# Kernel tuning notes

Measured on AMD Instinct MI355X. Metric: run time of the kernel, lower is better.

The kernel has to match this reference:

```python
import jax, jax.numpy as jnp
import numpy as np

NUM_ITERATIONS = 3
NUM_SLOTS = 8
SLOT_SIZE = 256
MLP_HIDDEN = 512
EPSILON = 1e-8
LN_EPS = 1e-5


def _ln(x, w, b):
    m = jnp.mean(x, axis=-1, keepdims=True)
    v = jnp.var(x, axis=-1, keepdims=True)
    return (x - m) * jax.lax.rsqrt(v + LN_EPS) * w + b


def _gru_cell(x, h, w_ih, w_hh, b_ih, b_hh):
    # torch.nn.GRUCell semantics; gates ordered [r, z, n]
    gi = x @ w_ih.T + b_ih
    gh = h @ w_hh.T + b_hh
    ir, iz, inn = jnp.split(gi, 3, axis=-1)
    hr, hz, hn = jnp.split(gh, 3, axis=-1)
    r = jax.nn.sigmoid(ir + hr)
    z = jax.nn.sigmoid(iz + hz)
    n = jnp.tanh(inn + r * hn)
    return (1.0 - z) * n + z * h


def setup_inputs() -> dict:
    key = jax.random.key(0)
    ks = jax.random.split(key, 12)
    D, H = SLOT_SIZE, MLP_HIDDEN
    s = 0.02
    return {
        "inputs": jax.random.normal(ks[0], (64, 4096, D), dtype=jnp.float32),
        "noise": jax.random.normal(ks[1], (64, NUM_SLOTS, D), dtype=jnp.float32),
        "ln_in_w": jnp.ones((D,), jnp.float32), "ln_in_b": jnp.zeros((D,), jnp.float32),
        "ln_slots_w": jnp.ones((D,), jnp.float32), "ln_slots_b": jnp.zeros((D,), jnp.float32),
        "ln_mlp_w": jnp.ones((D,), jnp.float32), "ln_mlp_b": jnp.zeros((D,), jnp.float32),
        "slots_mu": jax.random.normal(ks[2], (1, 1, D), jnp.float32) * s,
        "slots_log_sigma": jnp.zeros((1, 1, D), jnp.float32),
        "Wq": jax.random.normal(ks[3], (D, D), jnp.float32) * s,
        "Wk": jax.random.normal(ks[4], (D, D), jnp.float32) * s,
        "Wv": jax.random.normal(ks[5], (D, D), jnp.float32) * s,
        "gru_w_ih": jax.random.normal(ks[6], (3 * D, D), jnp.float32) * s,
        "gru_w_hh": jax.random.normal(ks[7], (3 * D, D), jnp.float32) * s,
        "gru_b_ih": jnp.zeros((3 * D,), jnp.float32),
        "gru_b_hh": jnp.zeros((3 * D,), jnp.float32),
        "mlp_w1": jax.random.normal(ks[8], (H, D), jnp.float32) * s,
        "mlp_b1": jnp.zeros((H,), jnp.float32),
        "mlp_w2": jax.random.normal(ks[9], (D, H), jnp.float32) * s,
        "mlp_b2": jnp.zeros((D,), jnp.float32),
    }


def reference(inputs, noise, ln_in_w, ln_in_b, ln_slots_w, ln_slots_b, ln_mlp_w, ln_mlp_b,
              slots_mu, slots_log_sigma, Wq, Wk, Wv,
              gru_w_ih, gru_w_hh, gru_b_ih, gru_b_hh,
              mlp_w1, mlp_b1, mlp_w2, mlp_b2):
    B, N, D = inputs.shape
    S = NUM_SLOTS
    x = _ln(inputs, ln_in_w, ln_in_b)            # [B,N,D]
    k = x @ Wk.T                                  # [B,N,D]
    v = x @ Wv.T                                  # [B,N,D]
    slots = slots_mu + jnp.exp(slots_log_sigma) * noise   # [B,S,D]
    scale = D ** (-0.5)
    for _ in range(NUM_ITERATIONS):
        slots_prev = slots
        s_n = _ln(slots, ln_slots_w, ln_slots_b)
        q = (s_n @ Wq.T) * scale                  # [B,S,D]
        attn_logits = jnp.einsum('bnd,bsd->bns', k, q)
        attn = jax.nn.softmax(attn_logits, axis=-1) + EPSILON
        attn = attn / jnp.sum(attn, axis=-2, keepdims=True)   # renorm over inputs
        updates = jnp.einsum('bns,bnd->bsd', attn, v)          # [B,S,D]
        slots = _gru_cell(updates.reshape(-1, D), slots_prev.reshape(-1, D),
                          gru_w_ih, gru_w_hh, gru_b_ih, gru_b_hh).reshape(B, S, D)
        h = jax.nn.relu(_ln(slots, ln_mlp_w, ln_mlp_b) @ mlp_w1.T + mlp_b1)
        slots = slots + (h @ mlp_w2.T + mlp_b2)
    return slots
```

## Files before the change

kernel.cpp:

```cpp
#include <hip/hip_runtime.h>

#define CB 64
#define CN 4096
#define CD 256
#define CS 8
#define CH 512

typedef __bf16 bf16_t;
typedef bf16_t bf16x8 __attribute__((ext_vector_type(8)));
typedef float f32x4 __attribute__((ext_vector_type(4)));

__device__ __forceinline__ unsigned short f2bf(float f){
  unsigned int u = __builtin_bit_cast(unsigned int, f);
  u += 0x7FFFu + ((u >> 16) & 1u);
  return (unsigned short)(u >> 16);
}

__device__ __forceinline__ f32x4 mfma16(bf16x8 a, bf16x8 b, f32x4 c){
  return __builtin_amdgcn_mfma_f32_16x16x32_bf16(a, b, c, 0, 0, 0);
}

__device__ __forceinline__ void gl_lds16(const void* g, void* l){
  __builtin_amdgcn_global_load_lds(
      (const __attribute__((address_space(1))) unsigned int*)g,
      (__attribute__((address_space(3))) unsigned int*)l, 16, 0, 0);
}

__global__ __launch_bounds__(256) void k_ln(const float* __restrict__ in,
    const float* __restrict__ gw, const float* __restrict__ gb,
    unsigned short* __restrict__ x){
  int blk = blockIdx.x;
  int b = blk >> 6, nt = blk & 63;
  int wv = threadIdx.x >> 6, l = threadIdx.x & 63;
  const float* base = in + ((size_t)b*CN + (size_t)nt*64) * CD;
  unsigned short* xb = x + ((size_t)b*CN + (size_t)nt*64) * CD;
  float4 w4 = *(const float4*)(gw + 4*l);
  float4 b4 = *(const float4*)(gb + 4*l);
  for(int i = 0; i < 16; i++){
    int r = wv*16 + i;
    float4 v = *(const float4*)(base + (size_t)r*CD + 4*l);
    float s1 = v.x + v.y + v.z + v.w;
    float s2 = v.x*v.x + v.y*v.y + v.z*v.z + v.w*v.w;
    #pragma unroll
    for(int m = 1; m < 64; m <<= 1){ s1 += __shfl_xor(s1, m); s2 += __shfl_xor(s2, m); }
    float mean = s1 * (1.0f/CD);
    float var  = fmaxf(s2 * (1.0f/CD) - mean*mean, 0.0f);
    float rstd = rsqrtf(var + 1e-5f);
    float y0 = (v.x - mean)*rstd*w4.x + b4.x;
    float y1 = (v.y - mean)*rstd*w4.y + b4.y;
    float y2 = (v.z - mean)*rstd*w4.z + b4.z;
    float y3 = (v.w - mean)*rstd*w4.w + b4.w;
    uint2 p;
    p.x = (unsigned)f2bf(y0) | ((unsigned)f2bf(y1) << 16);
    p.y = (unsigned)f2bf(y2) | ((unsigned)f2bf(y3) << 16);
    *(uint2*)(xb + (size_t)r*CD + 4*l) = p;
  }
}

__global__ __launch_bounds__(256) void k_setup(
    const float* __restrict__ Wq, const float* __restrict__ Wk,
    const float* __restrict__ wih, const float* __restrict__ Wv,
    const float* __restrict__ whh, const float* __restrict__ w1,
    const float* __restrict__ w2, const float* __restrict__ noise,
    const float* __restrict__ mu, const float* __restrict__ lsig,
    unsigned short* __restrict__ M1T, unsigned short* __restrict__ Mih_bf,
    unsigned short* __restrict__ Whh_bf, unsigned short* __restrict__ w1_bf,
    unsigned short* __restrict__ w2_bf, float* __restrict__ slots){
  int bid = blockIdx.x, tid = threadIdx.x;
  if(bid < 256){
    int ep = bid, e = tid;
    float acc = 0.0f;
    for(int d = 0; d < 256; d++) acc = fmaf(Wq[(size_t)d*256 + e], Wk[(size_t)d*256 + ep], acc);
    M1T[(size_t)ep*256 + e] = f2bf(acc * 0.0625f);
  } else if(bid < 1024){
    int j = bid - 256, e = tid;
    float acc = 0.0f;
    for(int d = 0; d < 256; d++) acc = fmaf(wih[(size_t)j*256 + d], Wv[(size_t)d*256 + e], acc);
    Mih_bf[(size_t)j*256 + e] = f2bf(acc);
  } else if(bid < 1792){
    int idx = (bid - 1024)*256 + tid;
    Whh_bf[idx] = f2bf(whh[idx]);
  } else if(bid < 2304){
    int idx = (bid - 1792)*256 + tid;
    w1_bf[idx] = f2bf(w1[idx]);
  } else if(bid < 2816){
    int idx = (bid - 2304)*256 + tid;
    w2_bf[idx] = f2bf(w2[idx]);
  } else {
    int idx = (bid - 2816)*256 + tid;
    int d = idx & 255;
    slots[idx] = mu[d] + __expf(lsig[d]) * noise[idx];
  }
}

__global__ __launch_bounds__(256) void k_attn(const unsigned short* __restrict__ x,
    const float* __restrict__ slots, const float* __restrict__ lsw,
    const float* __restrict__ lsb, const unsigned short* __restrict__ M1T,
    float* __restrict__ Upart, float* __restrict__ dpart){
  __shared__ unsigned short xt[64*256];
  __shared__ unsigned short pt[16*72];
  __shared__ float dred[4][8];
  int b = blockIdx.x >> 4, chunk = blockIdx.x & 15;
  int tid = threadIdx.x;
  int wv = tid >> 6, l = tid & 63;
  int lm = l & 15, lg = l >> 4;

  unsigned short* sn    = xt;
  unsigned short* qtile = xt + 4224;
  {
    float4 w4 = *(const float4*)(lsw + 4*l);
    float4 b4 = *(const float4*)(lsb + 4*l);
    for(int i = 0; i < 2; i++){
      int r = wv*2 + i;
      float4 v = *(const float4*)(slots + ((size_t)b*CS + r)*CD + 4*l);
      float s1 = v.x + v.y + v.z + v.w;
      float s2 = v.x*v.x + v.y*v.y + v.z*v.z + v.w*v.w;
      #pragma unroll
      for(int m = 1; m < 64; m <<= 1){ s1 += __shfl_xor(s1, m); s2 += __shfl_xor(s2, m); }
      float mean = s1 * (1.0f/CD);
      float var  = fmaxf(s2 * (1.0f/CD) - mean*mean, 0.0f);
      float rstd = rsqrtf(var + 1e-5f);
      float y0 = (v.x - mean)*rstd*w4.x + b4.x;
      float y1 = (v.y - mean)*rstd*w4.y + b4.y;
      float y2 = (v.z - mean)*rstd*w4.z + b4.z;
      float y3 = (v.w - mean)*rstd*w4.w + b4.w;
      uint2 p;
      p.x = (unsigned)f2bf(y0) | ((unsigned)f2bf(y1) << 16);
      p.y = (unsigned)f2bf(y2) | ((unsigned)f2bf(y3) << 16);
      *(uint2*)(&sn[r*264 + 4*l]) = p;
      uint2 zz; zz.x = 0u; zz.y = 0u;
      *(uint2*)(&sn[(r+8)*264 + 4*l]) = zz;
    }
    __syncthreads();
    bf16x8 af[8];
    #pragma unroll
    for(int k = 0; k < 8; k++) af[k] = *(const bf16x8*)(&sn[lm*264 + k*32 + lg*8]);
    #pragma unroll
    for(int ntile = 0; ntile < 4; ntile++){
      int ep = wv*64 + ntile*16 + lm;
      f32x4 acc = {0.f, 0.f, 0.f, 0.f};
      const unsigned short* mrow = M1T + (size_t)ep*CD;
      #pragma unroll
      for(int k = 0; k < 8; k++){
        bf16x8 bf = *(const bf16x8*)(mrow + k*32 + lg*8);
        acc = mfma16(af[k], bf, acc);
      }
      #pragma unroll
      for(int reg = 0; reg < 4; reg++)
        qtile[(lg*4 + reg)*264 + ep] = f2bf(acc[reg]);
    }
    __syncthreads();
  }
  bf16x8 qb[8];
  #pragma unroll
  for(int k = 0; k < 8; k++) qb[k] = *(const bf16x8*)(&qtile[lm*264 + k*32 + lg*8]);

  f32x4 uacc[4];
  #pragma unroll
  for(int nt = 0; nt < 4; nt++){ f32x4 z = {0.f,0.f,0.f,0.f}; uacc[nt] = z; }
  float dacc = 0.0f;

  const unsigned short* xbatch = x + (size_t)b*CN*CD + (size_t)chunk*256*CD;

  for(int t = 0; t < 4; t++){
    const unsigned short* xtile = xbatch + (size_t)t*64*CD;
    __syncthreads();
    #pragma unroll
    for(int k2 = 0; k2 < 8; k2++){
      int r0 = wv*16 + k2*2;
      int row = r0 + (l >> 5);
      int c = l & 31;
      int f = (row ^ (row >> 3)) & 7;
      const unsigned short* g = xtile + (size_t)row*CD + (size_t)(c ^ f)*8;
      gl_lds16(g, &xt[r0*CD]);
    }
    __syncthreads();

    f32x4 c4 = {0.f, 0.f, 0.f, 0.f};
    int rowl = wv*16 + lm;
    int f1 = (rowl ^ (rowl >> 3)) & 7;
    #pragma unroll
    for(int k = 0; k < 8; k++){
      int cc = (k*4 + lg) ^ f1;
      bf16x8 a = *(const bf16x8*)(&xt[rowl*256 + cc*8]);
      c4 = mfma16(a, qb[k], c4);
    }
    float pv[4];
    #pragma unroll
    for(int reg = 0; reg < 4; reg++){
      float v = (lm < 8) ? c4[reg] : -1e30f;
      float mx = v;
      #pragma unroll
      for(int m = 1; m < 16; m <<= 1) mx = fmaxf(mx, __shfl_xor(mx, m));
      float e = __expf(v - mx);
      float s = e;
      #pragma unroll
      for(int m = 1; m < 16; m <<= 1) s += __shfl_xor(s, m);
      float p = (lm < 8) ? (e/s + 1e-8f) : 0.0f;
      dacc += p;
      pv[reg] = p;
    }
    int rbase = wv*16 + lg*4;
    unsigned int p01 = (unsigned)f2bf(pv[0]) | ((unsigned)f2bf(pv[1]) << 16);
    unsigned int p23 = (unsigned)f2bf(pv[2]) | ((unsigned)f2bf(pv[3]) << 16);
    *(unsigned int*)(&pt[lm*72 + rbase])     = p01;
    *(unsigned int*)(&pt[lm*72 + rbase + 2]) = p23;
    __syncthreads();

    #pragma unroll
    for(int ks = 0; ks < 2; ks++){
      bf16x8 a = *(const bf16x8*)(&pt[lm*72 + ks*32 + lg*8]);
      int rb = ks*32 + lg*8;
      #pragma unroll
      for(int nt = 0; nt < 4; nt++){
        int e = wv*64 + nt*16 + lm;
        bf16x8 bfr;
        #pragma unroll
        for(int j = 0; j < 8; j++){
          int row2 = rb + j;
          int f2 = (row2 ^ (row2 >> 3)) & 7;
          int cidx = (e >> 3) ^ f2;
          unsigned short tv = xt[row2*256 + cidx*8 + (e & 7)];
          bfr[j] = __builtin_bit_cast(bf16_t, tv);
        }
        uacc[nt] = mfma16(a, bfr, uacc[nt]);
      }
    }
  }

  dacc += __shfl_xor(dacc, 16);
  dacc += __shfl_xor(dacc, 32);
  if(l < 8) dred[wv][l] = dacc;
  if(lg < 2){
    float* Ub = Upart + (((size_t)chunk*CB + b)*CS)*CD;
    #pragma unroll
    for(int nt = 0; nt < 4; nt++){
      #pragma unroll
      for(int reg = 0; reg < 4; reg++){
        int s = lg*4 + reg;
        Ub[(size_t)s*CD + wv*64 + nt*16 + lm] = uacc[nt][reg];
      }
    }
  }
  __syncthreads();
  if(tid < 8)
    dpart[((size_t)chunk*CB + b)*CS + tid] =
        dred[0][tid] + dred[1][tid] + dred[2][tid] + dred[3][tid];
}

__global__ __launch_bounds__(512) void k_update(
    const float* __restrict__ Upart, const float* slots,
    const float* __restrict__ dpart,
    const unsigned short* __restrict__ Mih, const unsigned short* __restrict__ Whh,
    const unsigned short* __restrict__ w1b, const unsigned short* __restrict__ w2b,
    const float* __restrict__ bih, const float* __restrict__ bhh,
    const float* __restrict__ lmw, const float* __restrict__ lmb,
    const float* __restrict__ b1, const float* __restrict__ b2,
    float* out){
  __shared__ unsigned short A1[16*264];
  __shared__ unsigned short SBf[16*264];
  __shared__ unsigned short A3[16*520];
  __shared__ float G1[8*777];
  __shared__ float G2[8*777];
  __shared__ float Hh[8*257];
  int b = blockIdx.x, tid = threadIdx.x;
  int l = tid & 63, lm = l & 15, lg = l >> 4;
  int wv = tid >> 6;

  for(int i = tid; i < 8*264; i += 512){ A1[8*264 + i] = 0; SBf[8*264 + i] = 0; }
  for(int i = tid; i < 8*520; i += 512) A3[8*520 + i] = 0;
  if(tid < 256){
    int r = tid >> 5, c = (tid & 31)*8;
    float s0=0.f,s1=0.f,s2=0.f,s3=0.f,s4=0.f,s5=0.f,s6=0.f,s7=0.f;
    #pragma unroll
    for(int ch = 0; ch < 16; ch++){
      const float* Up = Upart + (((size_t)ch*CB + b)*CS + r)*CD + c;
      float4 a0 = *(const float4*)Up;
      float4 a1 = *(const float4*)(Up + 4);
      s0 += a0.x; s1 += a0.y; s2 += a0.z; s3 += a0.w;
      s4 += a1.x; s5 += a1.y; s6 += a1.z; s7 += a1.w;
    }
    uint4 pk;
    pk.x = (unsigned)f2bf(s0) | ((unsigned)f2bf(s1) << 16);
    pk.y = (unsigned)f2bf(s2) | ((unsigned)f2bf(s3) << 16);
    pk.z = (unsigned)f2bf(s4) | ((unsigned)f2bf(s5) << 16);
    pk.w = (unsigned)f2bf(s6) | ((unsigned)f2bf(s7) << 16);
    *(uint4*)(&A1[r*264 + c]) = pk;
  } else {
    int t2 = tid & 255;
    int r = t2 >> 5, c = (t2 & 31)*8;
    const float* src = slots + ((size_t)b*CS + r)*CD + c;
    float4 a0 = *(const float4*)src, a1 = *(const float4*)(src + 4);
    uint4 pk;
    pk.x = (unsigned)f2bf(a0.x) | ((unsigned)f2bf(a0.y) << 16);
    pk.y = (unsigned)f2bf(a0.z) | ((unsigned)f2bf(a0.w) << 16);
    pk.z = (unsigned)f2bf(a1.x) | ((unsigned)f2bf(a1.y) << 16);
    pk.w = (unsigned)f2bf(a1.z) | ((unsigned)f2bf(a1.w) << 16);
    *(uint4*)(&SBf[r*264 + c]) = pk;
  }
  __syncthreads();

  {
    const unsigned short* W = (wv < 4) ? Mih : Whh;
    const unsigned short* As = (wv < 4) ? A1 : SBf;
    float* G = (wv < 4) ? G1 : G2;
    int w4 = wv & 3;
    bf16x8 af[8];
    #pragma unroll
    for(int k = 0; k < 8; k++) af[k] = *(const bf16x8*)(&As[lm*264 + k*32 + lg*8]);
    const unsigned short* brow = W + ((size_t)(w4*192 + lm))*CD + lg*8;
    bf16x8 bv[8], bw[8];
    #pragma unroll
    for(int k = 0; k < 8; k++) bv[k] = *(const bf16x8*)(brow + k*32);
    for(int t = 0; t < 12; t++){
      if(t < 11){
        const unsigned short* bn = brow + (size_t)(t + 1)*16*CD;
        #pragma unroll
        for(int k = 0; k < 8; k++) bw[k] = *(const bf16x8*)(bn + k*32);
      }
      f32x4 acc = {0.f,0.f,0.f,0.f};
      #pragma unroll
      for(int k = 0; k < 8; k++) acc = mfma16(af[k], bv[k], acc);
      if(lg < 2){
        int cb = w4*192 + t*16 + lm;
        #pragma unroll
        for(int reg = 0; reg < 4; reg++) G[(lg*4 + reg)*777 + cb] = acc[reg];
      }
      #pragma unroll
      for(int k = 0; k < 8; k++) bv[k] = bw[k];
    }
  }
  __syncthreads();

  {
    int r = wv;
    float dsum = dpart[((size_t)(l & 15)*CB + b)*CS + r];
    #pragma unroll
    for(int m = 1; m < 16; m <<= 1) dsum += __shfl_xor(dsum, m);
    float invd = 1.0f / dsum;
    const float* srow = slots + ((size_t)b*CS + r)*CD;
    float hv[4]; float s1 = 0.f, s2 = 0.f;
    #pragma unroll
    for(int i = 0; i < 4; i++){
      int c = l + 64*i;
      float gr = G1[r*777 + c]*invd + bih[c] + G2[r*777 + c] + bhh[c];
      float gz = G1[r*777 + 256 + c]*invd + bih[256 + c] + G2[r*777 + 256 + c] + bhh[256 + c];
      float gn = G1[r*777 + 512 + c]*invd + bih[512 + c];
      float hn = G2[r*777 + 512 + c] + bhh[512 + c];
      float rr = 1.0f/(1.0f + __expf(-gr));
      float zz = 1.0f/(1.0f + __expf(-gz));
      float nn = tanhf(gn + rr*hn);
      float h = (1.0f - zz)*nn + zz*srow[c];
      hv[i] = h; Hh[r*257 + c] = h; s1 += h; s2 += h*h;
    }
    #pragma unroll
    for(int m = 1; m < 64; m <<= 1){ s1 += __shfl_xor(s1, m); s2 += __shfl_xor(s2, m); }
    float mean = s1 * (1.0f/CD);
    float var  = fmaxf(s2 * (1.0f/CD) - mean*mean, 0.0f);
    float rstd = rsqrtf(var + 1e-5f);
    #pragma unroll
    for(int i = 0; i < 4; i++){
      int c = l + 64*i;
      A1[r*264 + c] = f2bf((hv[i] - mean)*rstd*lmw[c] + lmb[c]);
    }
  }
  __syncthreads();

  {
    bf16x8 af[8];
    #pragma unroll
    for(int k = 0; k < 8; k++) af[k] = *(const bf16x8*)(&A1[lm*264 + k*32 + lg*8]);
    const unsigned short* brow = w1b + ((size_t)(wv*64 + lm))*CD + lg*8;
    for(int t = 0; t < 4; t++){
      const unsigned short* bn = brow + (size_t)t*16*CD;
      f32x4 acc = {0.f,0.f,0.f,0.f};
      #pragma unroll
      for(int k = 0; k < 8; k++){
        bf16x8 bv = *(const bf16x8*)(bn + k*32);
        acc = mfma16(af[k], bv, acc);
      }
      if(lg < 2){
        int c = wv*64 + t*16 + lm;
        float bb = b1[c];
        #pragma unroll
        for(int reg = 0; reg < 4; reg++)
          A3[(lg*4 + reg)*520 + c] = f2bf(fmaxf(acc[reg] + bb, 0.0f));
      }
    }
  }
  __syncthreads();

  {
    bf16x8 af[16];
    #pragma unroll
    for(int k = 0; k < 16; k++) af[k] = *(const bf16x8*)(&A3[lm*520 + k*32 + lg*8]);
    const unsigned short* brow = w2b + ((size_t)(wv*32 + lm))*CH + lg*8;
    for(int t = 0; t < 2; t++){
      const unsigned short* bn = brow + (size_t)t*16*CH;
      f32x4 acc = {0.f,0.f,0.f,0.f};
      #pragma unroll
      for(int k = 0; k < 16; k++){
        bf16x8 bv = *(const bf16x8*)(bn + k*32);
        acc = mfma16(af[k], bv, acc);
      }
      if(lg < 2){
        int c = wv*32 + t*16 + lm;
        float bb = b2[c];
        #pragma unroll
        for(int reg = 0; reg < 4; reg++){
          int row = lg*4 + reg;
          out[((size_t)b*CS + row)*CD + c] = acc[reg] + bb + Hh[row*257 + c];
        }
      }
    }
  }
}

extern "C" void kernel_launch(void* const* d_in, const int* in_sizes, int n_in,
                              void* d_out, int out_size, void* d_ws, size_t ws_size,
                              hipStream_t stream){
  const float* inputs = (const float*)d_in[0];
  const float* noise  = (const float*)d_in[1];
  const float* ln_in_w = (const float*)d_in[2];
  const float* ln_in_b = (const float*)d_in[3];
  const float* ln_sl_w = (const float*)d_in[4];
  const float* ln_sl_b = (const float*)d_in[5];
  const float* ln_ml_w = (const float*)d_in[6];
  const float* ln_ml_b = (const float*)d_in[7];
  const float* mu   = (const float*)d_in[8];
  const float* lsig = (const float*)d_in[9];
  const float* Wq  = (const float*)d_in[10];
  const float* Wk  = (const float*)d_in[11];
  const float* Wv  = (const float*)d_in[12];
  const float* wih = (const float*)d_in[13];
  const float* whh = (const float*)d_in[14];
  const float* bih = (const float*)d_in[15];
  const float* bhh = (const float*)d_in[16];
  const float* w1  = (const float*)d_in[17];
  const float* b1  = (const float*)d_in[18];
  const float* w2  = (const float*)d_in[19];
  const float* b2  = (const float*)d_in[20];

  char* ws = (char*)d_ws;
  size_t off = 0;
  unsigned short* x = (unsigned short*)(ws + off); off += (size_t)CB*CN*CD*2;
  float* slots = (float*)(ws + off); off += (size_t)CB*CS*CD*4;
  float* Upart = (float*)(ws + off); off += (size_t)16*CB*CS*CD*4;
  float* dpart = (float*)(ws + off); off += (size_t)16*CB*CS*4;
  unsigned short* M1T    = (unsigned short*)(ws + off); off += (size_t)CD*CD*2;
  unsigned short* Mih_bf = (unsigned short*)(ws + off); off += (size_t)768*CD*2;
  unsigned short* Whh_bf = (unsigned short*)(ws + off); off += (size_t)768*CD*2;
  unsigned short* w1_bf  = (unsigned short*)(ws + off); off += (size_t)CH*CD*2;
  unsigned short* w2_bf  = (unsigned short*)(ws + off); off += (size_t)CD*CH*2;

  k_ln<<<4096, 256, 0, stream>>>(inputs, ln_in_w, ln_in_b, x);
  k_setup<<<3328, 256, 0, stream>>>(Wq, Wk, wih, Wv, whh, w1, w2, noise, mu, lsig,
                                    M1T, Mih_bf, Whh_bf, w1_bf, w2_bf, slots);

  for(int it = 0; it < 3; it++){
    k_attn<<<1024, 256, 0, stream>>>(x, slots, ln_sl_w, ln_sl_b, M1T, Upart, dpart);
    float* dst = (it == 2) ? (float*)d_out : slots;
    k_update<<<64, 512, 0, stream>>>(Upart, slots, dpart,
        Mih_bf, Whh_bf, w1_bf, w2_bf,
        bih, bhh, ln_ml_w, ln_ml_b, b1, b2, dst);
  }
}
```

Baseline: 680.1 us.

## Double-buffer input tiles and use transposed LDS reads for attention update

The attention kernel now keeps two LDS buffers and prefetches the next 64-row input tile with async global-to-LDS loads while the current tile is processed, using explicit vmcnt waits and raw barriers. The LDS layout is rearranged so the logits MFMA reads contiguous fragments. The scalar 8-element gather for the P·V B-operand is replaced with ds_read_b64_tr_b16 transposed reads. This removes load latency and many scalar LDS reads per tile, at the cost of doubled LDS usage (possible occupancy loss) and fragile hand-written waitcnt/barrier sequencing.

```diff
diff --git a/kernel.cpp b/kernel.cpp
--- a/kernel.cpp
+++ b/kernel.cpp
@@ -9,6 +9,8 @@
 typedef __bf16 bf16_t;
 typedef bf16_t bf16x8 __attribute__((ext_vector_type(8)));
 typedef float f32x4 __attribute__((ext_vector_type(4)));
+typedef unsigned long long u64;
+typedef u64 u64x2 __attribute__((ext_vector_type(2)));
 
 __device__ __forceinline__ unsigned short f2bf(float f){
   unsigned int u = __builtin_bit_cast(unsigned int, f);
@@ -97,7 +99,7 @@
     const float* __restrict__ slots, const float* __restrict__ lsw,
     const float* __restrict__ lsb, const unsigned short* __restrict__ M1T,
     float* __restrict__ Upart, float* __restrict__ dpart){
-  __shared__ unsigned short xt[64*256];
+  __shared__ unsigned short xb2[2][16384];
   __shared__ unsigned short pt[16*72];
   __shared__ float dred[4][8];
   int b = blockIdx.x >> 4, chunk = blockIdx.x & 15;
@@ -105,8 +107,8 @@
   int wv = tid >> 6, l = tid & 63;
   int lm = l & 15, lg = l >> 4;
 
-  unsigned short* sn    = xt;
-  unsigned short* qtile = xt + 4224;
+  unsigned short* sn    = &xb2[0][0];
+  unsigned short* qtile = &xb2[1][0];
   {
     float4 w4 = *(const float4*)(lsw + 4*l);
     float4 b4 = *(const float4*)(lsb + 4*l);
@@ -154,6 +156,9 @@
   bf16x8 qb[8];
   #pragma unroll
   for(int k = 0; k < 8; k++) qb[k] = *(const bf16x8*)(&qtile[lm*264 + k*32 + lg*8]);
+  asm volatile("s_waitcnt lgkmcnt(0)" ::: "memory");
+  __builtin_amdgcn_sched_barrier(0);
+  __builtin_amdgcn_s_barrier();
 
   f32x4 uacc[4];
   #pragma unroll
@@ -162,28 +167,36 @@
 
   const unsigned short* xbatch = x + (size_t)b*CN*CD + (size_t)chunk*256*CD;
 
+  #define STAGE(dstbuf, tptr) { \
+    const unsigned short* xt_ = (tptr); \
+    unsigned short* ld_ = (dstbuf) + wv*4096; \
+    _Pragma("unroll") \
+    for(int k2 = 0; k2 < 8; k2++){ \
+      int n_  = wv*16 + (k2>>1)*4 + ((l&7)>>1); \
+      int e0_ = ((k2&1)*8 + (l>>3))*16 + (l&1)*8; \
+      gl_lds16(xt_ + (size_t)n_*CD + e0_, ld_ + k2*512); \
+    } }
+
+  STAGE(&xb2[0][0], xbatch);
+
+  #pragma unroll
   for(int t = 0; t < 4; t++){
-    const unsigned short* xtile = xbatch + (size_t)t*64*CD;
-    __syncthreads();
-    #pragma unroll
-    for(int k2 = 0; k2 < 8; k2++){
-      int r0 = wv*16 + k2*2;
-      int row = r0 + (l >> 5);
-      int c = l & 31;
-      int f = (row ^ (row >> 3)) & 7;
-      const unsigned short* g = xtile + (size_t)row*CD + (size_t)(c ^ f)*8;
-      gl_lds16(g, &xt[r0*CD]);
-    }
-    __syncthreads();
-
+    if(t < 3) STAGE(&xb2[(t+1)&1][0], xbatch + (size_t)(t+1)*64*CD);
+    if(t < 3) asm volatile("s_waitcnt vmcnt(8)" ::: "memory");
+    else      asm volatile("s_waitcnt vmcnt(0)" ::: "memory");
+    __builtin_amdgcn_sched_barrier(0);
+    __builtin_amdgcn_s_barrier();
+    __builtin_amdgcn_sched_barrier(0);
+
+    const unsigned short* xcur = &xb2[t&1][0];
     f32x4 c4 = {0.f, 0.f, 0.f, 0.f};
-    int rowl = wv*16 + lm;
-    int f1 = (rowl ^ (rowl >> 3)) & 7;
-    #pragma unroll
-    for(int k = 0; k < 8; k++){
-      int cc = (k*4 + lg) ^ f1;
-      bf16x8 a = *(const bf16x8*)(&xt[rowl*256 + cc*8]);
-      c4 = mfma16(a, qb[k], c4);
+    {
+      int abase = wv*4096 + (lm>>2)*1024 + (lm&3)*16 + (lg>>1)*64 + (lg&1)*8;
+      #pragma unroll
+      for(int k = 0; k < 8; k++){
+        bf16x8 a = *(const bf16x8*)(xcur + abase + k*128);
+        c4 = mfma16(a, qb[k], c4);
+      }
     }
     float pv[4];
     #pragma unroll
@@ -205,28 +218,41 @@
     unsigned int p23 = (unsigned)f2bf(pv[2]) | ((unsigned)f2bf(pv[3]) << 16);
     *(unsigned int*)(&pt[lm*72 + rbase])     = p01;
     *(unsigned int*)(&pt[lm*72 + rbase + 2]) = p23;
-    __syncthreads();
-
-    #pragma unroll
-    for(int ks = 0; ks < 2; ks++){
-      bf16x8 a = *(const bf16x8*)(&pt[lm*72 + ks*32 + lg*8]);
-      int rb = ks*32 + lg*8;
+    asm volatile("s_waitcnt lgkmcnt(0)" ::: "memory");
+    __builtin_amdgcn_sched_barrier(0);
+    __builtin_amdgcn_s_barrier();
+    __builtin_amdgcn_sched_barrier(0);
+
+    {
+      bf16x8 aP0 = *(const bf16x8*)(&pt[lm*72 + lg*8]);
+      bf16x8 aP1 = *(const bf16x8*)(&pt[lm*72 + 32 + lg*8]);
+      unsigned xoff = (unsigned)(size_t)xcur;
+      unsigned bse = xoff + (unsigned)(lg*2*16*128 + wv*4*128 + lm*8);
+      u64 t0[4], t1[4], t2[4], t3[4];
       #pragma unroll
       for(int nt = 0; nt < 4; nt++){
-        int e = wv*64 + nt*16 + lm;
-        bf16x8 bfr;
-        #pragma unroll
-        for(int j = 0; j < 8; j++){
-          int row2 = rb + j;
-          int f2 = (row2 ^ (row2 >> 3)) & 7;
-          int cidx = (e >> 3) ^ f2;
-          unsigned short tv = xt[row2*256 + cidx*8 + (e & 7)];
-          bfr[j] = __builtin_bit_cast(bf16_t, tv);
-        }
-        uacc[nt] = mfma16(a, bfr, uacc[nt]);
-      }
-    }
-  }
+        unsigned a0 = bse + nt*128;
+        asm volatile("ds_read_b64_tr_b16 %0, %4\n\t"
+                     "ds_read_b64_tr_b16 %1, %4 offset:2048\n\t"
+                     "ds_read_b64_tr_b16 %2, %4 offset:16384\n\t"
+                     "ds_read_b64_tr_b16 %3, %4 offset:18432"
+                     : "=v"(t0[nt]), "=v"(t1[nt]), "=v"(t2[nt]), "=v"(t3[nt])
+                     : "v"(a0));
+      }
+      asm volatile("s_waitcnt lgkmcnt(0)" ::: "memory");
+      __builtin_amdgcn_sched_barrier(0);
+      #pragma unroll
+      for(int nt = 0; nt < 4; nt++){
+        u64x2 q0; q0[0] = t0[nt]; q0[1] = t1[nt];
+        u64x2 q1; q1[0] = t2[nt]; q1[1] = t3[nt];
+        uacc[nt] = mfma16(aP0, __builtin_bit_cast(bf16x8, q0), uacc[nt]);
+        uacc[nt] = mfma16(aP1, __builtin_bit_cast(bf16x8, q1), uacc[nt]);
+      }
+    }
+    __builtin_amdgcn_s_barrier();
+    __builtin_amdgcn_sched_barrier(0);
+  }
+  #undef STAGE
 
   dacc += __shfl_xor(dacc, 16);
   dacc += __shfl_xor(dacc, 32);
```

New measurement: 685.3 us. No clear change (+0.8%).
